# Optimization experiments

Hardware: AMD Instinct MI355X
Metric: run time of the kernel (lower is better)

Reference implementation:

```python
import jax, jax.numpy as jnp
import numpy as np
from jax import lax

K_NEIGH = 10


def setup_inputs() -> dict:
    key = jax.random.key(0)
    k1, k2, k3, k4, k5 = jax.random.split(key, 5)
    bs, C, T = 8, 256, 2048
    x = jax.random.normal(k1, (bs, C, T), dtype=jnp.float32)
    num_frms = jax.random.randint(k2, (bs,), 0, 2048)
    # Conv1d(in=C, out=C, kernel=3, pad=1): weight [out, in, k], bias [out]
    conv_w = jax.random.normal(k3, (C, C, 3), dtype=jnp.float32) * (1.0 / np.sqrt(3 * C))
    conv_b = jnp.zeros((C,), dtype=jnp.float32)
    # Linear(2*C -> C): weight [out, 2*in], bias [out]
    mlp_w = jax.random.normal(k4, (C, 2 * C), dtype=jnp.float32) * (1.0 / np.sqrt(2 * C))
    mlp_b = jax.random.normal(k5, (C,), dtype=jnp.float32) * 0.01
    return {"x": x, "num_frms": num_frms, "conv_w": conv_w, "conv_b": conv_b,
            "mlp_w": mlp_w, "mlp_b": mlp_b}


def _knn_idx(x, k):
    # x: [bs, C, T]; dif[b,i,j] = ||x[b,:,i] - x[b,:,j]||^2 via norm expansion
    sq = jnp.sum(x * x, axis=1)                      # [bs, T]
    gram = jnp.einsum('bci,bcj->bij', x, x)          # [bs, T, T]
    dif = sq[:, :, None] + sq[:, None, :] - 2.0 * gram
    _, idx = lax.top_k(-dif, k)                      # k smallest distances
    return idx                                       # [bs, T, k]


def reference(x, num_frms, conv_w, conv_b, mlp_w, mlp_b):
    bs, C, T = x.shape
    Cout = conv_w.shape[0]
    # temporal conv branch (kernel 3, stride 1, pad 1)
    c_out = lax.conv_general_dilated(
        x, conv_w, window_strides=(1,), padding=((1, 1),),
        dimension_numbers=('NCH', 'OIH', 'NCH')) + conv_b[None, :, None]
    # graph branch ('par': knn on x)
    idx = _knn_idx(x, K_NEIGH)                                   # [bs, T, k]
    idx_flat = (idx + jnp.arange(bs)[:, None, None] * T).reshape(-1, K_NEIGH)
    feat = x.transpose(0, 2, 1).reshape(bs * T, C)               # [N, C]
    feat_neigh = feat[idx_flat]                                  # [N, k, C]
    ctr = feat[:, None, :]                                       # [N, 1, C]
    cat = jnp.concatenate(
        [feat_neigh, jnp.broadcast_to(ctr, feat_neigh.shape)], axis=-1)  # [N,k,2C]
    g = jnp.einsum('nkc,oc->nko', cat, mlp_w) + mlp_b            # [N, k, Cout]
    # cosine edge weight
    num = jnp.einsum('nkc,nc->nk', feat_neigh, feat)
    den = jnp.sqrt(jnp.sum(feat_neigh * feat_neigh, axis=2)) * \
          jnp.sqrt(jnp.sum(feat * feat, axis=1))[:, None]
    w = num / den                                                # [N, k]
    g = g * w[:, :, None]
    g = jnp.max(g, axis=1)                                       # [N, Cout]
    g_out = g.reshape(bs, T, Cout).transpose(0, 2, 1)            # [bs, Cout, T]
    out = jax.nn.relu(c_out + g_out)
    # MaxPool1d(kernel=2, stride=2)
    out = out.reshape(bs, Cout, T // 2, 2).max(axis=-1)
    return out
```

## Files before the change

### kernel.cpp

```cpp
#include <hip/hip_runtime.h>
#include <hip/hip_bf16.h>
#include <cstdint>

#define T_DIM 2048
#define C_DIM 256
#define BS 8
#define NPTS (BS * T_DIM)
#define KNB 10

typedef __bf16 bf16x8 __attribute__((ext_vector_type(8)));
typedef float f32x4 __attribute__((ext_vector_type(4)));

#define AS1 __attribute__((address_space(1)))
#define AS3 __attribute__((address_space(3)))

__device__ __forceinline__ unsigned short f2bf_rn(float f) {
  unsigned u = __float_as_uint(f);
  unsigned r = (u + 0x7FFFu + ((u >> 16) & 1u)) >> 16;
  return (unsigned short)r;
}
__device__ __forceinline__ float bfbits2f(unsigned short h) {
  return __uint_as_float((unsigned)h << 16);
}
__device__ __forceinline__ __bf16 bfbits(unsigned short h) {
  return __builtin_bit_cast(__bf16, h);
}

__device__ __forceinline__ void stage_tile(const __bf16* __restrict__ src, size_t row0,
                                           int ld, int k0, __bf16* lds, int w, int l) {
  int kofs = ((l & 7) ^ (l >> 3)) * 8;
  const __bf16* g0 = src + (row0 + (size_t)(l >> 3)) * ld + k0 + kofs;
  __bf16* lbase = lds + (size_t)(w * 4) * 512;
#pragma unroll
  for (int q4 = 0; q4 < 4; ++q4) {
    __builtin_amdgcn_global_load_lds((AS1 void*)(g0 + (size_t)(w * 4 + q4) * 8 * ld),
                                     (AS3 void*)(lbase + q4 * 512), 16, 0, 0);
  }
}

__device__ __forceinline__ void stage_tile_conv(const __bf16* __restrict__ src, int m0,
                                                int k0in, const __bf16* __restrict__ zp,
                                                __bf16* lds, int w, int l) {
  int tap = k0in >> 8;
  int kshift = tap - 1;
  int k0 = k0in & 255;
  int kofs = ((l & 7) ^ (l >> 3)) * 8;
  int mb = m0 & (T_DIM - 1);
#pragma unroll
  for (int q4 = 0; q4 < 4; ++q4) {
    int q = w * 4 + q4;
    int row = q * 8 + (l >> 3);
    int t = mb + row + kshift;
    const __bf16* g = ((unsigned)t < (unsigned)T_DIM)
                          ? (src + (size_t)(m0 + row + kshift) * C_DIM + k0 + kofs)
                          : (zp + kofs);
    __builtin_amdgcn_global_load_lds((AS1 void*)g, (AS3 void*)(lds + q * 512), 16, 0, 0);
  }
}

__device__ __forceinline__ bf16x8 read_frag(const __bf16* lds, int t16, int ks, int l) {
  int row = t16 * 16 + (l & 15);
  int kb = ks * 64 + ((l >> 4) << 4);
  int byte = row * 128 + (kb ^ ((row & 7) << 4));
  return *(const bf16x8*)((const char*)lds + byte);
}

__global__ __launch_bounds__(256) void k_transpose_split(const float* __restrict__ x,
                                                         __bf16* __restrict__ Fh,
                                                         __bf16* __restrict__ Fl) {
  __shared__ float tile[32][33];
  int b = blockIdx.z;
  int t0 = blockIdx.x * 32;
  int c0 = blockIdx.y * 32;
  int tx = threadIdx.x & 31, ty = threadIdx.x >> 5;
  const float* xb = x + (size_t)b * C_DIM * T_DIM;
#pragma unroll
  for (int r = 0; r < 4; ++r) {
    int c = c0 + ty + 8 * r;
    tile[ty + 8 * r][tx] = xb[(size_t)c * T_DIM + t0 + tx];
  }
  __syncthreads();
#pragma unroll
  for (int r = 0; r < 4; ++r) {
    int t = t0 + ty + 8 * r;
    float v = tile[tx][ty + 8 * r];
    unsigned short hb = f2bf_rn(v);
    float lo = v - bfbits2f(hb);
    size_t o = ((size_t)b * T_DIM + t) * C_DIM + c0 + tx;
    Fh[o] = bfbits(hb);
    Fl[o] = bfbits(f2bf_rn(lo));
  }
}

__global__ __launch_bounds__(256) void k_sq(const __bf16* __restrict__ Fh,
                                            const __bf16* __restrict__ Fl,
                                            float* __restrict__ sq) {
  int n = blockIdx.x * 4 + (threadIdx.x >> 6);
  int lane = threadIdx.x & 63;
  ushort4 hv = ((const ushort4*)Fh)[(size_t)n * 64 + lane];
  ushort4 lv = ((const ushort4*)Fl)[(size_t)n * 64 + lane];
  float s = 0.f;
  {
    float v;
    v = bfbits2f(hv.x) + bfbits2f(lv.x); s = fmaf(v, v, s);
    v = bfbits2f(hv.y) + bfbits2f(lv.y); s = fmaf(v, v, s);
    v = bfbits2f(hv.z) + bfbits2f(lv.z); s = fmaf(v, v, s);
    v = bfbits2f(hv.w) + bfbits2f(lv.w); s = fmaf(v, v, s);
  }
#pragma unroll
  for (int d = 1; d < 64; d <<= 1) s += __shfl_xor(s, d, 64);
  if (lane == 0) sq[n] = s;
}

__global__ __launch_bounds__(256, 2) void k_gram_sym(const __bf16* __restrict__ Fh,
                                                     const __bf16* __restrict__ Fl,
                                                     float* __restrict__ gram) {
  __shared__ __align__(16) char smem[65536];
  __bf16* Ah = (__bf16*)smem;
  __bf16* Al = (__bf16*)(smem + 16384);
  __bf16* Bh = (__bf16*)(smem + 32768);
  __bf16* Bl = (__bf16*)(smem + 49152);

  int b = blockIdx.y;
  int ti = blockIdx.x;
  int by = (int)((sqrtf(8.0f * (float)ti + 1.0f) - 1.0f) * 0.5f);
  if ((by + 1) * (by + 2) / 2 <= ti) by++;
  int bx = ti - by * (by + 1) / 2;

  size_t base = (size_t)b * T_DIM;
  int m0 = by * 128, n0 = bx * 128;
  int tid = threadIdx.x, w = tid >> 6, l = tid & 63;
  int wr = w >> 1, wc = w & 1;
  f32x4 acc[4][4];
#pragma unroll
  for (int i = 0; i < 4; ++i)
#pragma unroll
    for (int j = 0; j < 4; ++j) acc[i][j] = {0.f, 0.f, 0.f, 0.f};

  for (int k0 = 0; k0 < C_DIM; k0 += 64) {
    stage_tile(Fh, base + m0, C_DIM, k0, Ah, w, l);
    stage_tile(Fl, base + m0, C_DIM, k0, Al, w, l);
    stage_tile(Fh, base + n0, C_DIM, k0, Bh, w, l);
    stage_tile(Fl, base + n0, C_DIM, k0, Bl, w, l);
    __syncthreads();
#pragma unroll
    for (int ks = 0; ks < 2; ++ks) {
      bf16x8 ah[4], bh[4], x[4];
#pragma unroll
      for (int i = 0; i < 4; ++i) ah[i] = read_frag(Ah, wr * 4 + i, ks, l);
#pragma unroll
      for (int j = 0; j < 4; ++j) bh[j] = read_frag(Bh, wc * 4 + j, ks, l);
#pragma unroll
      for (int i = 0; i < 4; ++i)
#pragma unroll
        for (int j = 0; j < 4; ++j)
          acc[i][j] = __builtin_amdgcn_mfma_f32_16x16x32_bf16(ah[i], bh[j], acc[i][j], 0, 0, 0);
#pragma unroll
      for (int i = 0; i < 4; ++i) x[i] = read_frag(Al, wr * 4 + i, ks, l);
#pragma unroll
      for (int i = 0; i < 4; ++i)
#pragma unroll
        for (int j = 0; j < 4; ++j)
          acc[i][j] = __builtin_amdgcn_mfma_f32_16x16x32_bf16(x[i], bh[j], acc[i][j], 0, 0, 0);
#pragma unroll
      for (int j = 0; j < 4; ++j) x[j] = read_frag(Bl, wc * 4 + j, ks, l);
#pragma unroll
      for (int i = 0; i < 4; ++i)
#pragma unroll
        for (int j = 0; j < 4; ++j)
          acc[i][j] = __builtin_amdgcn_mfma_f32_16x16x32_bf16(ah[i], x[j], acc[i][j], 0, 0, 0);
    }
    __syncthreads();
  }

  float* gout = gram + (size_t)b * T_DIM * T_DIM;
#pragma unroll
  for (int i = 0; i < 4; ++i) {
    int mrow = m0 + wr * 64 + i * 16 + ((l >> 4) << 2);
#pragma unroll
    for (int j = 0; j < 4; ++j) {
      int ncol = n0 + wc * 64 + j * 16 + (l & 15);
      float* cp = gout + (size_t)mrow * T_DIM + ncol;
#pragma unroll
      for (int r = 0; r < 4; ++r) cp[(size_t)r * T_DIM] = acc[i][j][r];
    }
  }

  if (bx != by) {
    float* Tbuf = (float*)smem;
#pragma unroll
    for (int h = 0; h < 2; ++h) {
      __syncthreads();
      if (wc == h) {
#pragma unroll
        for (int j = 0; j < 4; ++j) {
          int cH = j * 16 + (l & 15);
          float* dst = Tbuf + cH * 132 + wr * 64 + ((l >> 4) << 2);
#pragma unroll
          for (int i = 0; i < 4; ++i) *(f32x4*)(dst + i * 16) = acc[i][j];
        }
      }
      __syncthreads();
      int cH = tid >> 5;
      int c4 = (tid & 31) * 4;
#pragma unroll
      for (int p = 0; p < 8; ++p) {
        f32x4 v = *(const f32x4*)(Tbuf + (size_t)(p * 8 + cH) * 132 + c4);
        *(f32x4*)(gout + (size_t)(n0 + h * 64 + p * 8 + cH) * T_DIM + m0 + c4) = v;
      }
    }
  }
}

__global__ __launch_bounds__(256, 2) void k_gemm16(const __bf16* __restrict__ A,
                                                   const __bf16* __restrict__ Bm,
                                                   float* __restrict__ C, int N, int K,
                                                   int conv, const __bf16* __restrict__ zp) {
  __shared__ __bf16 As[128 * 64], Bs[128 * 64];
  int m0 = blockIdx.y * 128, n0 = blockIdx.x * 128;
  int tid = threadIdx.x, w = tid >> 6, l = tid & 63;
  int wr = w >> 1, wc = w & 1;
  f32x4 acc[4][4];
#pragma unroll
  for (int i = 0; i < 4; ++i)
#pragma unroll
    for (int j = 0; j < 4; ++j) acc[i][j] = {0.f, 0.f, 0.f, 0.f};

  for (int k0 = 0; k0 < K; k0 += 64) {
    if (conv)
      stage_tile_conv(A, m0, k0, zp, As, w, l);
    else
      stage_tile(A, (size_t)m0, C_DIM, k0, As, w, l);
    stage_tile(Bm, (size_t)n0, K, k0, Bs, w, l);
    __syncthreads();
#pragma unroll
    for (int ks = 0; ks < 2; ++ks) {
      bf16x8 af[4], bf_[4];
#pragma unroll
      for (int i = 0; i < 4; ++i) af[i] = read_frag(As, wr * 4 + i, ks, l);
#pragma unroll
      for (int j = 0; j < 4; ++j) bf_[j] = read_frag(Bs, wc * 4 + j, ks, l);
#pragma unroll
      for (int i = 0; i < 4; ++i)
#pragma unroll
        for (int j = 0; j < 4; ++j)
          acc[i][j] = __builtin_amdgcn_mfma_f32_16x16x32_bf16(af[i], bf_[j], acc[i][j], 0, 0, 0);
    }
    __syncthreads();
  }
#pragma unroll
  for (int i = 0; i < 4; ++i) {
    int mrow = m0 + wr * 64 + i * 16 + ((l >> 4) << 2);
#pragma unroll
    for (int j = 0; j < 4; ++j) {
      int ncol = n0 + wc * 64 + j * 16 + (l & 15);
      float* cp = C + (size_t)mrow * N + ncol;
#pragma unroll
      for (int r = 0; r < 4; ++r) cp[(size_t)r * N] = acc[i][j][r];
    }
  }
}

__global__ __launch_bounds__(256) void k_topk(const float* __restrict__ gram,
                                              const float* __restrict__ sq,
                                              int* __restrict__ idxo,
                                              float* __restrict__ wo) {
  int lb = blockIdx.y;
  const float* gramb = gram + (size_t)lb * T_DIM * T_DIM;
  const float* sqb = sq + (size_t)lb * T_DIM;
  int* idxb = idxo + (size_t)lb * T_DIM * KNB;
  float* wbp = wo + (size_t)lb * T_DIM * KNB;

  int row = blockIdx.x * 4 + (threadIdx.x >> 6);
  int lane = threadIdx.x & 63;
  float sqi = sqb[row];
  const float* g = gramb + (size_t)row * T_DIM;
  unsigned long long a0 = ~0ull, a1 = ~0ull, a2 = ~0ull, a3 = ~0ull, a4 = ~0ull,
                     a5 = ~0ull, a6 = ~0ull, a7 = ~0ull, a8 = ~0ull, a9 = ~0ull;
  for (int j = lane; j < T_DIM; j += 64) {
    float dif = sqi + sqb[j] - 2.0f * g[j];
    unsigned u = __float_as_uint(dif);
    u = (u & 0x80000000u) ? ~u : (u | 0x80000000u);
    unsigned long long key = ((unsigned long long)u << 32) | (unsigned)j;
    if (key < a9) {
      a9 = key;
      unsigned long long t;
      if (a9 < a8) { t = a8; a8 = a9; a9 = t; }
      if (a8 < a7) { t = a7; a7 = a8; a8 = t; }
      if (a7 < a6) { t = a6; a6 = a7; a7 = t; }
      if (a6 < a5) { t = a5; a5 = a6; a6 = t; }
      if (a5 < a4) { t = a4; a4 = a5; a5 = t; }
      if (a4 < a3) { t = a3; a3 = a4; a4 = t; }
      if (a3 < a2) { t = a2; a2 = a3; a3 = t; }
      if (a2 < a1) { t = a1; a1 = a2; a2 = t; }
      if (a1 < a0) { t = a0; a0 = a1; a1 = t; }
    }
  }
#pragma unroll
  for (int s = 0; s < KNB; ++s) {
    unsigned long long h = a0;
    unsigned long long m = h;
#pragma unroll
    for (int d = 1; d < 64; d <<= 1) {
      unsigned long long o = __shfl_xor(m, d, 64);
      m = (o < m) ? o : m;
    }
    unsigned long long bal = __ballot(h == m);
    int leader = (int)__builtin_ctzll(bal);
    if (lane == leader) {
      a0 = a1; a1 = a2; a2 = a3; a3 = a4; a4 = a5;
      a5 = a6; a6 = a7; a7 = a8; a8 = a9; a9 = ~0ull;
    }
    if (lane == 0) {
      int j = (int)(unsigned)(m & 0xffffffffull);
      unsigned su = (unsigned)(m >> 32);
      unsigned bits = (su & 0x80000000u) ? (su & 0x7fffffffu) : ~su;
      float dif = __uint_as_float(bits);
      float sqj = sqb[j];
      float num = 0.5f * (sqi + sqj - dif);
      float wv = num / (sqrtf(sqi) * sqrtf(sqj));
      idxb[row * KNB + s] = j;
      wbp[row * KNB + s] = wv;
    }
  }
}

__global__ __launch_bounds__(256) void k_gfinal(const float* __restrict__ mlpout,
                                                const float* __restrict__ mlp_b,
                                                const int* __restrict__ idxo,
                                                const float* __restrict__ wo,
                                                const float* __restrict__ convb,
                                                const float* __restrict__ cb,
                                                float* __restrict__ out) {
  __shared__ float tile[32][33];
  __shared__ int sj[64][KNB];
  __shared__ float sw[64][KNB];
  int b = blockIdx.z, c0 = blockIdx.y * 32, t20 = blockIdx.x * 32;
  int tid = threadIdx.x;
  int nbase = b * T_DIM + t20 * 2;
  for (int e = tid; e < 64 * KNB; e += 256) {
    int ln = e / KNB, k = e - ln * KNB;
    sj[ln][k] = b * T_DIM + idxo[(size_t)(nbase + ln) * KNB + k];
    sw[ln][k] = wo[(size_t)(nbase + ln) * KNB + k];
  }
  __syncthreads();
  int tx = tid & 31, ty = tid >> 5;
  int c = c0 + tx;
  float bias_c = cb[c];
  float mbias = mlp_b[c];
#pragma unroll
  for (int rr = 0; rr < 4; ++rr) {
    int lt2 = ty + 8 * rr;
    float res[2];
#pragma unroll
    for (int s = 0; s < 2; ++s) {
      int ln = 2 * lt2 + s;
      int n = nbase + ln;
      float q = mlpout[(size_t)n * 512 + 256 + c] + mbias;
      float mx = -3.4e38f;
#pragma unroll
      for (int k = 0; k < KNB; ++k) {
        float v = (mlpout[(size_t)sj[ln][k] * 512 + c] + q) * sw[ln][k];
        mx = fmaxf(mx, v);
      }
      float v = convb[(size_t)n * C_DIM + c] + mx + bias_c;
      res[s] = fmaxf(v, 0.f);
    }
    tile[lt2][tx] = fmaxf(res[0], res[1]);
  }
  __syncthreads();
#pragma unroll
  for (int rr = 0; rr < 4; ++rr) {
    int cc = c0 + ty + 8 * rr;
    out[((size_t)b * C_DIM + cc) * (T_DIM / 2) + t20 + tx] = tile[tx][ty + 8 * rr];
  }
}

__global__ void k_repack(const float* __restrict__ cw, const float* __restrict__ mw,
                         __bf16* __restrict__ wk3, __bf16* __restrict__ mlpB,
                         __bf16* __restrict__ zp) {
  int i = blockIdx.x * 256 + threadIdx.x;
  if (i < 3 * C_DIM * C_DIM) {
    int o = i / 768;
    int rem = i - o * 768;
    int tap = rem >> 8;
    int ii = rem & 255;
    wk3[i] = bfbits(f2bf_rn(cw[(size_t)o * 768 + ii * 3 + tap]));
  } else {
    int m = i - 3 * C_DIM * C_DIM;
    if (m < 512 * 256) {
      int r = m >> 8;
      int col = m & 255;
      mlpB[m] = bfbits(f2bf_rn(mw[(size_t)(r & 255) * 512 + ((r >> 8) << 8) + col]));
    }
  }
  if (blockIdx.x == 0 && threadIdx.x < 128) zp[threadIdx.x] = bfbits(0);
}

extern "C" void kernel_launch(void* const* d_in, const int* in_sizes, int n_in,
                              void* d_out, int out_size, void* d_ws, size_t ws_size,
                              hipStream_t stream) {
  const float* x = (const float*)d_in[0];
  const float* conv_w = (const float*)d_in[2];
  const float* conv_b = (const float*)d_in[3];
  const float* mlp_w = (const float*)d_in[4];
  const float* mlp_b = (const float*)d_in[5];
  float* out = (float*)d_out;

  char* ws = (char*)d_ws;
  size_t off = 0;
  auto alloc = [&](size_t bytes) -> void* {
    void* p = ws + off;
    off += (bytes + 255) & ~(size_t)255;
    return p;
  };
  float* gram = (float*)alloc((size_t)BS * T_DIM * T_DIM * 4);
  __bf16* Fh = (__bf16*)alloc((size_t)NPTS * C_DIM * 2);
  __bf16* Fl = (__bf16*)alloc((size_t)NPTS * C_DIM * 2);
  float* convout = (float*)alloc((size_t)NPTS * C_DIM * 4);
  float* mlpout = (float*)alloc((size_t)NPTS * 512 * 4);
  float* sq = (float*)alloc((size_t)NPTS * 4);
  int* idxb = (int*)alloc((size_t)NPTS * KNB * 4);
  float* wb = (float*)alloc((size_t)NPTS * KNB * 4);
  __bf16* wk3 = (__bf16*)alloc((size_t)3 * C_DIM * C_DIM * 2);
  __bf16* mlpB = (__bf16*)alloc((size_t)512 * 256 * 2);
  __bf16* zp = (__bf16*)alloc(512);

  k_repack<<<dim3(1280), 256, 0, stream>>>(conv_w, mlp_w, wk3, mlpB, zp);
  k_transpose_split<<<dim3(T_DIM / 32, C_DIM / 32, BS), 256, 0, stream>>>(x, Fh, Fl);
  k_sq<<<dim3(NPTS / 4), 256, 0, stream>>>(Fh, Fl, sq);

  k_gram_sym<<<dim3(136, BS), 256, 0, stream>>>(Fh, Fl, gram);
  k_topk<<<dim3(T_DIM / 4, BS), 256, 0, stream>>>(gram, sq, idxb, wb);

  k_gemm16<<<dim3(512 / 128, NPTS / 128), 256, 0, stream>>>(Fh, mlpB, mlpout, 512, 256, 0, zp);
  k_gemm16<<<dim3(256 / 128, NPTS / 128), 256, 0, stream>>>(Fh, wk3, convout, 256, 768, 1, zp);

  k_gfinal<<<dim3((T_DIM / 2) / 32, C_DIM / 32, BS), 256, 0, stream>>>(
      mlpout, mlp_b, idxb, wb, convout, conv_b, out);
}
```

Before: 197.6 us.

## Use per-lane top-2 fast path with exact fallback in kNN top-k

```diff
diff --git a/kernel.cpp b/kernel.cpp
--- a/kernel.cpp
+++ b/kernel.cpp
@@ -275,41 +275,93 @@
   int lane = threadIdx.x & 63;
   float sqi = sqb[row];
   const float* g = gramb + (size_t)row * T_DIM;
-  unsigned long long a0 = ~0ull, a1 = ~0ull, a2 = ~0ull, a3 = ~0ull, a4 = ~0ull,
-                     a5 = ~0ull, a6 = ~0ull, a7 = ~0ull, a8 = ~0ull, a9 = ~0ull;
-  for (int j = lane; j < T_DIM; j += 64) {
+
+  unsigned kh[32];
+  unsigned long long a0 = ~0ull, a1 = ~0ull;
+#pragma unroll
+  for (int t = 0; t < 32; ++t) {
+    int j = lane + 64 * t;
     float dif = sqi + sqb[j] - 2.0f * g[j];
     unsigned u = __float_as_uint(dif);
     u = (u & 0x80000000u) ? ~u : (u | 0x80000000u);
+    kh[t] = u;
     unsigned long long key = ((unsigned long long)u << 32) | (unsigned)j;
-    if (key < a9) {
-      a9 = key;
-      unsigned long long t;
-      if (a9 < a8) { t = a8; a8 = a9; a9 = t; }
-      if (a8 < a7) { t = a7; a7 = a8; a8 = t; }
-      if (a7 < a6) { t = a6; a6 = a7; a7 = t; }
-      if (a6 < a5) { t = a5; a5 = a6; a6 = t; }
-      if (a5 < a4) { t = a4; a4 = a5; a5 = t; }
-      if (a4 < a3) { t = a3; a3 = a4; a4 = t; }
-      if (a3 < a2) { t = a2; a2 = a3; a3 = t; }
-      if (a2 < a1) { t = a1; a1 = a2; a2 = t; }
-      if (a1 < a0) { t = a0; a0 = a1; a1 = t; }
-    }
-  }
+    unsigned long long mx = (key > a0) ? key : a0;
+    a0 = (key < a0) ? key : a0;
+    a1 = (mx < a1) ? mx : a1;
+  }
+
+  unsigned long long theta = 0;
 #pragma unroll
   for (int s = 0; s < KNB; ++s) {
-    unsigned long long h = a0;
-    unsigned long long m = h;
+    unsigned long long m = a0;
 #pragma unroll
     for (int d = 1; d < 64; d <<= 1) {
       unsigned long long o = __shfl_xor(m, d, 64);
       m = (o < m) ? o : m;
     }
-    unsigned long long bal = __ballot(h == m);
+    unsigned long long bal = __ballot(a0 == m);
+    int leader = (int)__builtin_ctzll(bal);
+    if (lane == leader) { a0 = a1; a1 = ~0ull; }
+    if (lane == 0) {
+      int j = (int)(unsigned)(m & 0xffffffffull);
+      unsigned su = (unsigned)(m >> 32);
+      unsigned bits = (su & 0x80000000u) ? (su & 0x7fffffffu) : ~su;
+      float dif = __uint_as_float(bits);
+      float sqj = sqb[j];
+      float num = 0.5f * (sqi + sqj - dif);
+      float wv = num / (sqrtf(sqi) * sqrtf(sqj));
+      idxb[row * KNB + s] = j;
+      wbp[row * KNB + s] = wv;
+    }
+    theta = m;
+  }
+
+  unsigned thi = (unsigned)(theta >> 32);
+  unsigned tlo = (unsigned)(theta & 0xffffffffull);
+  int c = 0;
+#pragma unroll
+  for (int t = 0; t < 32; ++t) {
+    unsigned j = (unsigned)(lane + 64 * t);
+    c += (kh[t] < thi) || ((kh[t] == thi) && (j < tlo));
+  }
+#pragma unroll
+  for (int d = 1; d < 64; d <<= 1) c += __shfl_xor(c, d, 64);
+
+  if (c == 9) return;
+
+  unsigned long long b0 = ~0ull, b1 = ~0ull, b2 = ~0ull, b3 = ~0ull, b4 = ~0ull,
+                     b5 = ~0ull, b6 = ~0ull, b7 = ~0ull, b8 = ~0ull, b9 = ~0ull;
+#pragma unroll
+  for (int t = 0; t < 32; ++t) {
+    unsigned long long key = ((unsigned long long)kh[t] << 32) | (unsigned)(lane + 64 * t);
+    if (key < b9) {
+      b9 = key;
+      unsigned long long tt;
+      if (b9 < b8) { tt = b8; b8 = b9; b9 = tt; }
+      if (b8 < b7) { tt = b7; b7 = b8; b8 = tt; }
+      if (b7 < b6) { tt = b6; b6 = b7; b7 = tt; }
+      if (b6 < b5) { tt = b5; b5 = b6; b6 = tt; }
+      if (b5 < b4) { tt = b4; b4 = b5; b5 = tt; }
+      if (b4 < b3) { tt = b3; b3 = b4; b4 = tt; }
+      if (b3 < b2) { tt = b2; b2 = b3; b3 = tt; }
+      if (b2 < b1) { tt = b1; b1 = b2; b2 = tt; }
+      if (b1 < b0) { tt = b0; b0 = b1; b1 = tt; }
+    }
+  }
+#pragma unroll
+  for (int s = 0; s < KNB; ++s) {
+    unsigned long long m = b0;
+#pragma unroll
+    for (int d = 1; d < 64; d <<= 1) {
+      unsigned long long o = __shfl_xor(m, d, 64);
+      m = (o < m) ? o : m;
+    }
+    unsigned long long bal = __ballot(b0 == m);
     int leader = (int)__builtin_ctzll(bal);
     if (lane == leader) {
-      a0 = a1; a1 = a2; a2 = a3; a3 = a4; a4 = a5;
-      a5 = a6; a6 = a7; a7 = a8; a8 = a9; a9 = ~0ull;
+      b0 = b1; b1 = b2; b2 = b3; b3 = b4; b4 = b5;
+      b5 = b6; b6 = b7; b7 = b8; b8 = b9; b9 = ~0ull;
     }
     if (lane == 0) {
       int j = (int)(unsigned)(m & 0xffffffffull);
```

Result: faster. 189.4 us (-4.2%).
